# Optimization experiments

Measured on AMD Instinct MI355X. Metric: run time of the kernel, lower is better.

Reference implementation:

```python
import jax, jax.numpy as jnp
import numpy as np

D_MODEL = 1024
NUM_HEADS = 16
D_K = D_MODEL // NUM_HEADS


def setup_inputs() -> dict:
    key = jax.random.key(0)
    ks = jax.random.split(key, 9)
    B, S = 4, 2048
    s = 1.0 / np.sqrt(D_MODEL)
    inp = {
        "x": jax.random.normal(ks[0], (B, S, D_MODEL), dtype=jnp.float32),
        "wq": jax.random.uniform(ks[1], (D_MODEL, D_MODEL), jnp.float32, -s, s),
        "bq": jax.random.uniform(ks[2], (D_MODEL,), jnp.float32, -s, s),
        "wk": jax.random.uniform(ks[3], (D_MODEL, D_MODEL), jnp.float32, -s, s),
        "bk": jax.random.uniform(ks[4], (D_MODEL,), jnp.float32, -s, s),
        "wv": jax.random.uniform(ks[5], (D_MODEL, D_MODEL), jnp.float32, -s, s),
        "bv": jax.random.uniform(ks[6], (D_MODEL,), jnp.float32, -s, s),
        "wo": jax.random.uniform(ks[7], (D_MODEL, D_MODEL), jnp.float32, -s, s),
        "bo": jax.random.uniform(ks[8], (D_MODEL,), jnp.float32, -s, s),
    }
    return inp


def reference(x, wq, bq, wk, bk, wv, bv, wo, bo):
    B, S, _ = x.shape
    H, Dk = NUM_HEADS, D_K
    # QKV projections; weights stored as (in, out) so y = x @ w + b
    q = (x @ wq + bq).reshape(B, S, H, Dk).transpose(0, 2, 1, 3)  # (B,H,S,Dk)
    k = (x @ wk + bk).reshape(B, S, H, Dk).transpose(0, 2, 1, 3)
    v = (x @ wv + bv).reshape(B, S, H, Dk).transpose(0, 2, 1, 3)
    scores = jnp.einsum("bhqd,bhkd->bhqk", q, k) / jnp.sqrt(jnp.float32(Dk))
    causal = jnp.tril(jnp.ones((S, S), dtype=bool))  # True = keep
    scores = jnp.where(causal, scores, jnp.float32(-jnp.inf))
    attn = jax.nn.softmax(scores, axis=-1)  # dropout=0 (eval)
    out = jnp.einsum("bhqk,bhkd->bhqd", attn, v)
    out = out.transpose(0, 2, 1, 3).reshape(B, S, H * Dk)
    return out @ wo + bo
```

## Files before the change

kernel.cpp:

```cpp
#include <hip/hip_runtime.h>
#include <hip/hip_bf16.h>


#define D_MODEL 1024
#define NHEADS  16
#define DK      64
#define BATCH   4
#define SEQ     2048
#define MROWS   (BATCH*SEQ)

typedef short bvec8 __attribute__((ext_vector_type(8)));
typedef float fvec4  __attribute__((ext_vector_type(4)));
typedef float fvec16 __attribute__((ext_vector_type(16)));

__device__ __forceinline__ unsigned short f2bf(float f) {
    unsigned int x = __float_as_uint(f);
    x += 0x7fffu + ((x >> 16) & 1u);
    return (unsigned short)(x >> 16);
}
__device__ __forceinline__ float bf2f(unsigned short u) {
    return __uint_as_float(((unsigned int)u) << 16);
}

__device__ __forceinline__ unsigned pack_bf16x2(float a, float b) {
#if __has_builtin(__builtin_amdgcn_cvt_pk_bf16_f32)
    typedef __bf16 bf16x2_t __attribute__((ext_vector_type(2)));
    union { bf16x2_t v; unsigned u; } cv;
    cv.v = __builtin_amdgcn_cvt_pk_bf16_f32(a, b);
    return cv.u;
#else
    return (unsigned)f2bf(a) | ((unsigned)f2bf(b) << 16);
#endif
}

__device__ __forceinline__ float fast_exp2(float x) {
#if __has_builtin(__builtin_amdgcn_exp2f)
    return __builtin_amdgcn_exp2f(x);
#else
    return exp2f(x);
#endif
}


__global__ void f32_to_bf16_k(const float* __restrict__ in,
                              unsigned short* __restrict__ out, int n4) {
    int i = blockIdx.x * 256 + threadIdx.x;
    if (i < n4) {
        float4 v = ((const float4*)in)[i];
        ushort4 o;
        o.x = f2bf(v.x); o.y = f2bf(v.y); o.z = f2bf(v.z); o.w = f2bf(v.w);
        ((ushort4*)out)[i] = o;
    }
}

__global__ void transpose_all_k(const float* __restrict__ wq, const float* __restrict__ wk,
                                const float* __restrict__ wv, const float* __restrict__ wo,
                                unsigned short* __restrict__ wqkvt,
                                unsigned short* __restrict__ wot) {
    __shared__ float tile[32][33];
    const int z = blockIdx.z;
    const float* W = (z == 0) ? wq : (z == 1) ? wk : (z == 2) ? wv : wo;
    unsigned short* Wt = (z == 3) ? wot : wqkvt + (size_t)z * D_MODEL * D_MODEL;
    int n0 = blockIdx.x * 32, k0 = blockIdx.y * 32;
    int tx = threadIdx.x & 31;
    int ty = (threadIdx.x >> 5) * 4;
#pragma unroll
    for (int i = 0; i < 4; ++i)
        tile[ty + i][tx] = W[(k0 + ty + i) * D_MODEL + n0 + tx];
    __syncthreads();
#pragma unroll
    for (int i = 0; i < 4; ++i)
        Wt[(n0 + ty + i) * D_MODEL + k0 + tx] = f2bf(tile[tx][ty + i]);
}

__global__ void build_cbias_k(const float* __restrict__ bq, const float* __restrict__ bk,
                              const float* __restrict__ bv, float* __restrict__ cb) {
    int i = blockIdx.x * 256 + threadIdx.x;
    float v = (i < 1024) ? bq[i] : (i < 2048) ? bk[i - 1024] : bv[i - 2048];
    cb[i] = v;
}

__global__ __launch_bounds__(256, 5)
void gemm_glds(const unsigned short* __restrict__ A,
               const unsigned short* __restrict__ Bt,
               const float* __restrict__ bias,
               unsigned short* __restrict__ oq,
               unsigned short* __restrict__ ok,
               unsigned short* __restrict__ ov,
               float* __restrict__ of,
               float qscale, int mode) {
    __shared__ __align__(16) unsigned short As[2][128 * 32];
    __shared__ __align__(16) unsigned short Bs[2][128 * 32];

    const int tid  = threadIdx.x;
    const int lane = tid & 63;
    const int w    = tid >> 6;
    const int wr   = w >> 1, wc = w & 1;
    const int quad = lane >> 4, l16 = lane & 15;

    const unsigned nwg = gridDim.x * gridDim.y;
    unsigned f = blockIdx.y * gridDim.x + blockIdx.x;
    f = (f & 7) * (nwg >> 3) + (f >> 3);
    const int rowBlock = (f / gridDim.x) * 128;
    const int colBlock = (f % gridDim.x) * 128;

    const int srow = tid >> 2;
    const int gc   = (tid & 3) ^ ((tid >> 3) & 3);

#define G_STAGE(KOFF, BUF) do {                                               \
    const unsigned short* a0_ =                                               \
        &A[(size_t)(rowBlock + srow) * D_MODEL + (KOFF) + gc * 8];            \
    const unsigned short* b0_ =                                               \
        &Bt[(size_t)(colBlock + srow) * D_MODEL + (KOFF) + gc * 8];           \
    __builtin_amdgcn_global_load_lds(                                         \
        (const __attribute__((address_space(1))) void*)a0_,                   \
        (__attribute__((address_space(3))) void*)&As[BUF][tid * 8], 16, 0, 0); \
    __builtin_amdgcn_global_load_lds(                                         \
        (const __attribute__((address_space(1))) void*)(a0_ + (size_t)64 * D_MODEL), \
        (__attribute__((address_space(3))) void*)&As[BUF][(tid + 256) * 8], 16, 0, 0); \
    __builtin_amdgcn_global_load_lds(                                         \
        (const __attribute__((address_space(1))) void*)b0_,                   \
        (__attribute__((address_space(3))) void*)&Bs[BUF][tid * 8], 16, 0, 0); \
    __builtin_amdgcn_global_load_lds(                                         \
        (const __attribute__((address_space(1))) void*)(b0_ + (size_t)64 * D_MODEL), \
        (__attribute__((address_space(3))) void*)&Bs[BUF][(tid + 256) * 8], 16, 0, 0); \
} while (0)

    fvec4 acc[4][4] = {};
    const int sw = quad ^ ((l16 >> 1) & 3);

    G_STAGE(0, 0);

    for (int i = 0; i < 32; ++i) {
        __syncthreads();
        const int buf = i & 1;
        if (i < 31) G_STAGE((i + 1) * 32, buf ^ 1);
        bvec8 af[4], bfr[4];
#pragma unroll
        for (int ii = 0; ii < 4; ++ii) {
            const int r = wr * 64 + ii * 16 + l16;
            af[ii] = *(const bvec8*)&As[buf][r * 32 + sw * 8];
        }
#pragma unroll
        for (int j = 0; j < 4; ++j) {
            const int r = wc * 64 + j * 16 + l16;
            bfr[j] = *(const bvec8*)&Bs[buf][r * 32 + sw * 8];
        }
#pragma unroll
        for (int ii = 0; ii < 4; ++ii)
#pragma unroll
            for (int j = 0; j < 4; ++j)
                acc[ii][j] = __builtin_amdgcn_mfma_f32_16x16x32_bf16(
                    af[ii], bfr[j], acc[ii][j], 0, 0, 0);
    }
#undef G_STAGE

    if (mode == 0) {
#pragma unroll
        for (int i = 0; i < 4; ++i) {
#pragma unroll
            for (int j = 0; j < 4; ++j) {
                int ncol = colBlock + wc * 64 + j * 16 + l16;
                int which = ncol >> 10;
                int nn = ncol & 1023;
                int h = nn >> 6, d = nn & 63;
                float bv = bias[ncol];
#pragma unroll
                for (int r = 0; r < 4; ++r) {
                    int mrow = rowBlock + wr * 64 + i * 16 + quad * 4 + r;
                    int b = mrow >> 11, s = mrow & (SEQ - 1);
                    float v = acc[i][j][r] + bv;
                    if (which == 0)
                        oq[(((b * NHEADS + h) * SEQ + s) * DK) + d] = f2bf(v * qscale);
                    else if (which == 1)
                        ok[(((b * NHEADS + h) * SEQ + s) * DK) + d] = f2bf(v);
                    else
                        ov[(((b * NHEADS + h) * DK + d) * SEQ) + s] = f2bf(v);
                }
            }
        }
    } else {
#pragma unroll
        for (int i = 0; i < 4; ++i) {
#pragma unroll
            for (int j = 0; j < 4; ++j) {
                int ncol = colBlock + wc * 64 + j * 16 + l16;
                float bv = bias[ncol];
#pragma unroll
                for (int r = 0; r < 4; ++r) {
                    int mrow = rowBlock + wr * 64 + i * 16 + quad * 4 + r;
                    of[(size_t)mrow * D_MODEL + ncol] = acc[i][j][r] + bv;
                }
            }
        }
    }
}

__global__ __launch_bounds__(256, 4)
void attn_mfmaA(const unsigned short* __restrict__ Q,
                const unsigned short* __restrict__ K,
                const unsigned short* __restrict__ Vt,
                unsigned short* __restrict__ O,
                unsigned short* __restrict__ Opart,
                float* __restrict__ Lpart) {
    __shared__ __align__(16) unsigned short Ksm[2][64 * 64];
    __shared__ __align__(16) unsigned short Vsm[2][64 * 64];
    __shared__ float Lsh[4][32];

    const int tid  = threadIdx.x;
    const int lane = tid & 63;
    const int wq   = tid >> 6;
    const int hf   = lane >> 5;
    const int l32  = lane & 31;

    unsigned f = (blockIdx.z * 16 + blockIdx.y) * 24 + blockIdx.x;
    f = (f & 7) * 192 + (f >> 3);
    const int bx = f % 24;
    const int hh = (f / 24) & 15;
    const int b  = f / 384;
    const int hb = b * NHEADS + hh;

    static const int qt_tbl[24] = {15,15,7,14,14,6,13,13,12,12,5,11,
                                   11,10,10,4,9,9,8,8,3,2,1,0};
    static const int md_tbl[24] = {0,1,2,0,1,2,0,1,0,1,2,0,
                                   1,0,1,2,0,1,0,1,2,2,2,2};
    const int qt = qt_tbl[bx];
    const int md = md_tbl[bx];
    const bool part = (md < 2);
    const int kt0 = (md == 1) ? qt + 1 : 0;
    const int kt1 = (md == 0) ? qt + 1 : 2 * qt + 2;
    const int slot = part ? ((qt - 8) * 2 + md) : 0;

    const size_t bhq = ((size_t)hb) * SEQ * DK;
    const unsigned short* Qb = Q + bhq;
    const unsigned short* Kb = K + bhq;
    const unsigned short* Vb = Vt + bhq;

    const int q0 = qt * 128 + wq * 32;

    bvec8 qf[4];
#pragma unroll
    for (int kc = 0; kc < 4; ++kc)
        qf[kc] = *(const bvec8*)&Qb[(q0 + l32) * DK + kc * 16 + hf * 8];

    const int r1 = tid >> 3;
    const int lcs = (tid & 7) ^ (r1 & 7);

#define ATTN_STAGE(KT, NB) do {                                               \
    const unsigned short* kg_ = Kb + ((KT) * 64 + r1) * DK + lcs * 8;         \
    const unsigned short* vg_ = Vb + (size_t)r1 * SEQ + (KT) * 64 + lcs * 8;  \
    __builtin_amdgcn_global_load_lds(                                         \
        (const __attribute__((address_space(1))) void*)kg_,                   \
        (__attribute__((address_space(3))) void*)&Ksm[NB][wq * 512], 16, 0, 0); \
    __builtin_amdgcn_global_load_lds(                                         \
        (const __attribute__((address_space(1))) void*)(kg_ + 32 * DK),       \
        (__attribute__((address_space(3))) void*)&Ksm[NB][2048 + wq * 512], 16, 0, 0); \
    __builtin_amdgcn_global_load_lds(                                         \
        (const __attribute__((address_space(1))) void*)vg_,                   \
        (__attribute__((address_space(3))) void*)&Vsm[NB][wq * 512], 16, 0, 0); \
    __builtin_amdgcn_global_load_lds(                                         \
        (const __attribute__((address_space(1))) void*)(vg_ + 32 * SEQ),      \
        (__attribute__((address_space(3))) void*)&Vsm[NB][2048 + wq * 512], 16, 0, 0); \
} while (0)

    const int ktact = 2 * qt + (wq >> 1);
    const int mofs  = (wq & 1) << 5;

    ATTN_STAGE(kt0, 0);

    fvec16 acc0 = {};
    fvec16 acc1 = {};
    float lp = 0.f;

    for (int kt = kt0; kt < kt1; ++kt) {
        __syncthreads();
        const int buf = (kt - kt0) & 1;
        if (kt + 1 < kt1)
            ATTN_STAGE(kt + 1, buf ^ 1);
        if (kt <= ktact) {
            const unsigned short* Kbuf = &Ksm[buf][0];
            const unsigned short* Vbuf = &Vsm[buf][0];

            fvec16 s0 = {}, s1 = {};
            __builtin_amdgcn_s_setprio(1);
#pragma unroll
            for (int kc = 0; kc < 4; ++kc) {
                const int ch = (((kc * 2 + hf) ^ (l32 & 7)) * 8);
                bvec8 a0 = *(const bvec8*)&Kbuf[l32 * 64 + ch];
                bvec8 a1 = *(const bvec8*)&Kbuf[(32 + l32) * 64 + ch];
                s0 = __builtin_amdgcn_mfma_f32_32x32x16_bf16(a0, qf[kc], s0, 0, 0, 0);
                s1 = __builtin_amdgcn_mfma_f32_32x32x16_bf16(a1, qf[kc], s1, 0, 0, 0);
            }
            __builtin_amdgcn_s_setprio(0);

            if (kt == ktact) {
#pragma unroll
                for (int r = 0; r < 16; ++r) {
                    const int key0 = (r & 3) + 8 * (r >> 2) + 4 * hf - mofs;
                    if (key0 > l32)      s0[r] = -__builtin_inff();
                    if (key0 + 32 > l32) s1[r] = -__builtin_inff();
                }
            }

            unsigned pk[16];
#pragma unroll
            for (int m = 0; m < 8; ++m) {
                float p0 = fast_exp2(s0[2 * m]);
                float p1 = fast_exp2(s0[2 * m + 1]);
                float p2 = fast_exp2(s1[2 * m]);
                float p3 = fast_exp2(s1[2 * m + 1]);
                lp += (p0 + p1) + (p2 + p3);
                pk[m]     = pack_bf16x2(p0, p1);
                pk[8 + m] = pack_bf16x2(p2, p3);
            }

            __builtin_amdgcn_s_setprio(1);
#pragma unroll
            for (int kc16 = 0; kc16 < 4; ++kc16) {
                const int b0 = (kc16 >> 1) * 8 + (kc16 & 1) * 4;
                union { unsigned u[4]; bvec8 v; } afu;
#if __has_builtin(__builtin_amdgcn_permlane32_swap)
                {
                    auto r02 = __builtin_amdgcn_permlane32_swap(
                        pk[b0 + 0], pk[b0 + 2], false, false);
                    auto r13 = __builtin_amdgcn_permlane32_swap(
                        pk[b0 + 1], pk[b0 + 3], false, false);
                    unsigned o02[2], o13[2];
                    __builtin_memcpy(o02, &r02, 8);
                    __builtin_memcpy(o13, &r13, 8);
                    afu.u[0] = o02[0]; afu.u[2] = o02[1];
                    afu.u[1] = o13[0]; afu.u[3] = o13[1];
                }
#else
                {
                    unsigned sw0 = __shfl_xor(pk[b0 + 0], 32);
                    unsigned sw1 = __shfl_xor(pk[b0 + 1], 32);
                    unsigned sw2 = __shfl_xor(pk[b0 + 2], 32);
                    unsigned sw3 = __shfl_xor(pk[b0 + 3], 32);
                    afu.u[0] = hf ? sw2 : pk[b0 + 0];
                    afu.u[1] = hf ? sw3 : pk[b0 + 1];
                    afu.u[2] = hf ? pk[b0 + 2] : sw0;
                    afu.u[3] = hf ? pk[b0 + 3] : sw1;
                }
#endif
                const int ch = (((kc16 * 2 + hf) ^ (l32 & 7)) * 8);
                bvec8 bv0 = *(const bvec8*)&Vbuf[l32 * 64 + ch];
                bvec8 bv1 = *(const bvec8*)&Vbuf[(32 + l32) * 64 + ch];
                acc0 = __builtin_amdgcn_mfma_f32_32x32x16_bf16(afu.v, bv0, acc0, 0, 0, 0);
                acc1 = __builtin_amdgcn_mfma_f32_32x32x16_bf16(afu.v, bv1, acc1, 0, 0, 0);
            }
            __builtin_amdgcn_s_setprio(0);
        }
    }
#undef ATTN_STAGE

    const float l = lp + __shfl_xor(lp, 32);

    if (part) {
        if (lane < 32)
            Lpart[((size_t)slot * 64 + hb) * 128 + wq * 32 + l32] = l;
        unsigned short* Od = Opart + (((size_t)slot * 64 + hb) * 128 + wq * 32) * 64;
#pragma unroll
        for (int g = 0; g < 4; ++g)
#pragma unroll
            for (int rr = 0; rr < 4; ++rr) {
                const int reg = g * 4 + rr;
                const int qrl = g * 8 + 4 * hf + rr;
                Od[(size_t)qrl * 64 + l32]      = f2bf(acc0[reg]);
                Od[(size_t)qrl * 64 + 32 + l32] = f2bf(acc1[reg]);
            }
    } else {
        if (lane < 32) Lsh[wq][l32] = l;
#pragma unroll
        for (int g = 0; g < 4; ++g) {
            float4 lv = *(const float4*)&Lsh[wq][g * 8 + 4 * hf];
#pragma unroll
            for (int rr = 0; rr < 4; ++rr) {
                const int reg = g * 4 + rr;
                const int qrow = q0 + g * 8 + 4 * hf + rr;
                const float inv = 1.f / ((const float*)&lv)[rr];
                unsigned short* dst = O + (size_t)(b * SEQ + qrow) * D_MODEL + hh * DK + l32;
                dst[0]  = f2bf(acc0[reg] * inv);
                dst[32] = f2bf(acc1[reg] * inv);
            }
        }
    }
}

__global__ void attn_combine_k(const unsigned short* __restrict__ Opart,
                               const float* __restrict__ Lpart,
                               unsigned short* __restrict__ O) {
    const int qt = 8 + blockIdx.x;
    const int h = blockIdx.y, b = blockIdx.z;
    const int hb = b * NHEADS + h;
    const int s0 = (qt - 8) * 2;
    const unsigned short* A  = Opart + ((size_t)(s0)*64 + hb) * 128 * 64;
    const unsigned short* Bp = Opart + ((size_t)(s0 + 1) * 64 + hb) * 128 * 64;
    const float* LA = Lpart + ((size_t)(s0)*64 + hb) * 128;
    const float* LB = Lpart + ((size_t)(s0 + 1) * 64 + hb) * 128;
    for (int e = threadIdx.x; e < 128 * 64; e += 256) {
        const int qr = e >> 6, d = e & 63;
        const float inv = 1.f / (LA[qr] + LB[qr]);
        const float v = (bf2f(A[e]) + bf2f(Bp[e])) * inv;
        O[(size_t)(b * SEQ + qt * 128 + qr) * D_MODEL + h * DK + d] = f2bf(v);
    }
}


extern "C" void kernel_launch(void* const* d_in, const int* in_sizes, int n_in,
                              void* d_out, int out_size, void* d_ws, size_t ws_size,
                              hipStream_t stream) {
    const float* x  = (const float*)d_in[0];
    const float* wq = (const float*)d_in[1];
    const float* bq = (const float*)d_in[2];
    const float* wk = (const float*)d_in[3];
    const float* bk = (const float*)d_in[4];
    const float* wv = (const float*)d_in[5];
    const float* bv = (const float*)d_in[6];
    const float* wo = (const float*)d_in[7];
    const float* bo = (const float*)d_in[8];
    float* out = (float*)d_out;

    char* ws = (char*)d_ws;
    const size_t MB = 1u << 20;
    unsigned short* xb    = (unsigned short*)(ws);
    unsigned short* wqkvt = (unsigned short*)(ws + 16 * MB);
    unsigned short* wot   = (unsigned short*)(ws + 22 * MB);
    unsigned short* qb    = (unsigned short*)(ws + 24 * MB);
    unsigned short* kb    = (unsigned short*)(ws + 40 * MB);
    unsigned short* vtb   = (unsigned short*)(ws + 56 * MB);
    unsigned short* ab    = (unsigned short*)(ws + 72 * MB);
    float* cbias = (float*)(ws + 72 * MB);
    unsigned short* Opart = (unsigned short*)(ws);
    float* Lpart = (float*)(ws + 16 * MB);

    f32_to_bf16_k<<<(MROWS * D_MODEL / 4 + 255) / 256, 256, 0, stream>>>(
        x, xb, MROWS * D_MODEL / 4);
    transpose_all_k<<<dim3(32, 32, 4), 256, 0, stream>>>(wq, wk, wv, wo, wqkvt, wot);
    build_cbias_k<<<12, 256, 0, stream>>>(bq, bk, bv, cbias);

    const float QSCALE = 0.125f * 1.44269504088896340736f;

    gemm_glds<<<dim3(3072 / 128, MROWS / 128), 256, 0, stream>>>(
        xb, wqkvt, cbias, qb, kb, vtb, nullptr, QSCALE, 0);

    attn_mfmaA<<<dim3(24, NHEADS, BATCH), 256, 0, stream>>>(
        qb, kb, vtb, ab, Opart, Lpart);
    attn_combine_k<<<dim3(8, NHEADS, BATCH), 256, 0, stream>>>(Opart, Lpart, ab);

    gemm_glds<<<dim3(D_MODEL / 128, MROWS / 128), 256, 0, stream>>>(
        ab, wot, bo, nullptr, nullptr, nullptr, out, 1.0f, 1);
}
```

Before: 305.8 us.

## Deepen GEMM LDS pipeline to four stages and vectorize V-store and combine

Changes the projection GEMM from a double-buffered to a four-buffer LDS pipeline. Three tiles are prefetched via global_load_lds, and explicit vmcnt waits plus s_barrier replace __syncthreads. The transposed V output is now written as packed ushort4 along the sequence dimension instead of scattered scalar stores. The attention combine kernel is vectorized to process four elements per thread. The extra LDS (64KB) lowers the occupancy bound from 5 to 2 blocks per CU, which trades latency hiding across blocks for latency hiding within one block.

```diff
diff --git a/kernel.cpp b/kernel.cpp
--- a/kernel.cpp
+++ b/kernel.cpp
@@ -80,7 +80,7 @@
     cb[i] = v;
 }
 
-__global__ __launch_bounds__(256, 5)
+__global__ __launch_bounds__(256, 2)
 void gemm_glds(const unsigned short* __restrict__ A,
                const unsigned short* __restrict__ Bt,
                const float* __restrict__ bias,
@@ -89,8 +89,8 @@
                unsigned short* __restrict__ ov,
                float* __restrict__ of,
                float qscale, int mode) {
-    __shared__ __align__(16) unsigned short As[2][128 * 32];
-    __shared__ __align__(16) unsigned short Bs[2][128 * 32];
+    __shared__ __align__(16) unsigned short As[4][128 * 32];
+    __shared__ __align__(16) unsigned short Bs[4][128 * 32];
 
     const int tid  = threadIdx.x;
     const int lane = tid & 63;
@@ -106,54 +106,66 @@
 
     const int srow = tid >> 2;
     const int gc   = (tid & 3) ^ ((tid >> 3) & 3);
-
-#define G_STAGE(KOFF, BUF) do {                                               \
-    const unsigned short* a0_ =                                               \
-        &A[(size_t)(rowBlock + srow) * D_MODEL + (KOFF) + gc * 8];            \
-    const unsigned short* b0_ =                                               \
-        &Bt[(size_t)(colBlock + srow) * D_MODEL + (KOFF) + gc * 8];           \
-    __builtin_amdgcn_global_load_lds(                                         \
-        (const __attribute__((address_space(1))) void*)a0_,                   \
-        (__attribute__((address_space(3))) void*)&As[BUF][tid * 8], 16, 0, 0); \
-    __builtin_amdgcn_global_load_lds(                                         \
-        (const __attribute__((address_space(1))) void*)(a0_ + (size_t)64 * D_MODEL), \
-        (__attribute__((address_space(3))) void*)&As[BUF][(tid + 256) * 8], 16, 0, 0); \
-    __builtin_amdgcn_global_load_lds(                                         \
-        (const __attribute__((address_space(1))) void*)b0_,                   \
-        (__attribute__((address_space(3))) void*)&Bs[BUF][tid * 8], 16, 0, 0); \
-    __builtin_amdgcn_global_load_lds(                                         \
-        (const __attribute__((address_space(1))) void*)(b0_ + (size_t)64 * D_MODEL), \
-        (__attribute__((address_space(3))) void*)&Bs[BUF][(tid + 256) * 8], 16, 0, 0); \
+    const size_t abase = (size_t)(rowBlock + srow) * D_MODEL + gc * 8;
+    const size_t bbase = (size_t)(colBlock + srow) * D_MODEL + gc * 8;
+    const size_t rstep = (size_t)64 * D_MODEL;
+
+#define G_STAGE(T) do {                                                       \
+    const int _b = (T) & 3; const int _k = (T) * 32;                          \
+    __builtin_amdgcn_global_load_lds(                                         \
+        (const __attribute__((address_space(1))) void*)(A + abase + _k),      \
+        (__attribute__((address_space(3))) void*)&As[_b][tid * 8], 16, 0, 0); \
+    __builtin_amdgcn_global_load_lds(                                         \
+        (const __attribute__((address_space(1))) void*)(A + abase + rstep + _k), \
+        (__attribute__((address_space(3))) void*)&As[_b][(tid + 256) * 8], 16, 0, 0); \
+    __builtin_amdgcn_global_load_lds(                                         \
+        (const __attribute__((address_space(1))) void*)(Bt + bbase + _k),     \
+        (__attribute__((address_space(3))) void*)&Bs[_b][tid * 8], 16, 0, 0); \
+    __builtin_amdgcn_global_load_lds(                                         \
+        (const __attribute__((address_space(1))) void*)(Bt + bbase + rstep + _k), \
+        (__attribute__((address_space(3))) void*)&Bs[_b][(tid + 256) * 8], 16, 0, 0); \
+} while (0)
+
+#define G_COMPUTE(I) do {                                                     \
+    const int _buf = (I) & 3;                                                 \
+    bvec8 af[4], bfr[4];                                                      \
+    _Pragma("unroll")                                                         \
+    for (int ii = 0; ii < 4; ++ii) {                                          \
+        const int r = wr * 64 + ii * 16 + l16;                                \
+        af[ii] = *(const bvec8*)&As[_buf][r * 32 + sw * 8];                   \
+    }                                                                         \
+    _Pragma("unroll")                                                         \
+    for (int j = 0; j < 4; ++j) {                                             \
+        const int r = wc * 64 + j * 16 + l16;                                 \
+        bfr[j] = *(const bvec8*)&Bs[_buf][r * 32 + sw * 8];                   \
+    }                                                                         \
+    _Pragma("unroll")                                                         \
+    for (int ii = 0; ii < 4; ++ii)                                            \
+        _Pragma("unroll")                                                     \
+        for (int j = 0; j < 4; ++j)                                           \
+            acc[ii][j] = __builtin_amdgcn_mfma_f32_16x16x32_bf16(             \
+                af[ii], bfr[j], acc[ii][j], 0, 0, 0);                         \
 } while (0)
 
     fvec4 acc[4][4] = {};
     const int sw = quad ^ ((l16 >> 1) & 3);
 
-    G_STAGE(0, 0);
-
-    for (int i = 0; i < 32; ++i) {
-        __syncthreads();
-        const int buf = i & 1;
-        if (i < 31) G_STAGE((i + 1) * 32, buf ^ 1);
-        bvec8 af[4], bfr[4];
-#pragma unroll
-        for (int ii = 0; ii < 4; ++ii) {
-            const int r = wr * 64 + ii * 16 + l16;
-            af[ii] = *(const bvec8*)&As[buf][r * 32 + sw * 8];
-        }
-#pragma unroll
-        for (int j = 0; j < 4; ++j) {
-            const int r = wc * 64 + j * 16 + l16;
-            bfr[j] = *(const bvec8*)&Bs[buf][r * 32 + sw * 8];
-        }
-#pragma unroll
-        for (int ii = 0; ii < 4; ++ii)
-#pragma unroll
-            for (int j = 0; j < 4; ++j)
-                acc[ii][j] = __builtin_amdgcn_mfma_f32_16x16x32_bf16(
-                    af[ii], bfr[j], acc[ii][j], 0, 0, 0);
-    }
+    G_STAGE(0); G_STAGE(1); G_STAGE(2);
+
+    for (int i = 0; i < 29; ++i) {
+        asm volatile("s_waitcnt vmcnt(8)\n\ts_barrier" ::: "memory");
+        G_STAGE(i + 3);
+        G_COMPUTE(i);
+    }
+    asm volatile("s_waitcnt vmcnt(8)\n\ts_barrier" ::: "memory");
+    G_COMPUTE(29);
+    asm volatile("s_waitcnt vmcnt(4)\n\ts_barrier" ::: "memory");
+    G_COMPUTE(30);
+    asm volatile("s_waitcnt vmcnt(0)\n\ts_barrier" ::: "memory");
+    G_COMPUTE(31);
+
 #undef G_STAGE
+#undef G_COMPUTE
 
     if (mode == 0) {
 #pragma unroll
@@ -165,17 +177,26 @@
                 int nn = ncol & 1023;
                 int h = nn >> 6, d = nn & 63;
                 float bv = bias[ncol];
-#pragma unroll
-                for (int r = 0; r < 4; ++r) {
-                    int mrow = rowBlock + wr * 64 + i * 16 + quad * 4 + r;
-                    int b = mrow >> 11, s = mrow & (SEQ - 1);
-                    float v = acc[i][j][r] + bv;
-                    if (which == 0)
-                        oq[(((b * NHEADS + h) * SEQ + s) * DK) + d] = f2bf(v * qscale);
-                    else if (which == 1)
-                        ok[(((b * NHEADS + h) * SEQ + s) * DK) + d] = f2bf(v);
-                    else
-                        ov[(((b * NHEADS + h) * DK + d) * SEQ) + s] = f2bf(v);
+                if (which == 2) {
+                    const int mrow0 = rowBlock + wr * 64 + i * 16 + quad * 4;
+                    const int b = mrow0 >> 11, s0 = mrow0 & (SEQ - 1);
+                    ushort4 pv;
+                    pv.x = f2bf(acc[i][j][0] + bv);
+                    pv.y = f2bf(acc[i][j][1] + bv);
+                    pv.z = f2bf(acc[i][j][2] + bv);
+                    pv.w = f2bf(acc[i][j][3] + bv);
+                    *(ushort4*)&ov[(((size_t)(b * NHEADS + h) * DK + d) * SEQ) + s0] = pv;
+                } else {
+#pragma unroll
+                    for (int r = 0; r < 4; ++r) {
+                        int mrow = rowBlock + wr * 64 + i * 16 + quad * 4 + r;
+                        int b = mrow >> 11, s = mrow & (SEQ - 1);
+                        float v = acc[i][j][r] + bv;
+                        if (which == 0)
+                            oq[(((b * NHEADS + h) * SEQ + s) * DK) + d] = f2bf(v * qscale);
+                        else
+                            ok[(((b * NHEADS + h) * SEQ + s) * DK) + d] = f2bf(v);
+                    }
                 }
             }
         }
@@ -398,11 +419,17 @@
     const unsigned short* Bp = Opart + ((size_t)(s0 + 1) * 64 + hb) * 128 * 64;
     const float* LA = Lpart + ((size_t)(s0)*64 + hb) * 128;
     const float* LB = Lpart + ((size_t)(s0 + 1) * 64 + hb) * 128;
-    for (int e = threadIdx.x; e < 128 * 64; e += 256) {
-        const int qr = e >> 6, d = e & 63;
+    for (int e4 = threadIdx.x; e4 < 2048; e4 += 256) {
+        const int qr = e4 >> 4, d4 = (e4 & 15) * 4;
         const float inv = 1.f / (LA[qr] + LB[qr]);
-        const float v = (bf2f(A[e]) + bf2f(Bp[e])) * inv;
-        O[(size_t)(b * SEQ + qt * 128 + qr) * D_MODEL + h * DK + d] = f2bf(v);
+        ushort4 a = *(const ushort4*)&A[(size_t)qr * 64 + d4];
+        ushort4 p = *(const ushort4*)&Bp[(size_t)qr * 64 + d4];
+        ushort4 o;
+        o.x = f2bf((bf2f(a.x) + bf2f(p.x)) * inv);
+        o.y = f2bf((bf2f(a.y) + bf2f(p.y)) * inv);
+        o.z = f2bf((bf2f(a.z) + bf2f(p.z)) * inv);
+        o.w = f2bf((bf2f(a.w) + bf2f(p.w)) * inv);
+        *(ushort4*)&O[(size_t)(b * SEQ + qt * 128 + qr) * D_MODEL + h * DK + d4] = o;
     }
 }
 
```

Result: faster. 278.7 us (-8.9%).
